# Kernel tuning notes

Hardware: AMD Instinct MI355X
Metric: run time of the kernel (lower is better)

## Reference

```python
import jax, jax.numpy as jnp
import numpy as np

N_EMBED = 768
NUM_HEADS = 12
HEAD_SIZE = N_EMBED // NUM_HEADS
EPS = 1e-6


def layer_norm(x, gamma, beta):
    # torch .var() is unbiased (ddof=1)
    mean = x.mean(-1, keepdims=True)
    var = jnp.var(x, axis=-1, keepdims=True, ddof=1)
    xhat = (x - mean) / jnp.sqrt(var + EPS)
    return gamma * xhat + beta


def setup_inputs() -> dict:
    key = jax.random.key(0)
    ks = jax.random.split(key, 10)
    B, S, D = 4, 2048, N_EMBED
    H = 4 * D
    s = 0.02
    return {
        "x": jax.random.normal(ks[0], (B, S, D), jnp.float32),
        "wq": jax.random.normal(ks[1], (D, D), jnp.float32) * s,
        "wk": jax.random.normal(ks[2], (D, D), jnp.float32) * s,
        "wv": jax.random.normal(ks[3], (D, D), jnp.float32) * s,
        "wo": jax.random.normal(ks[4], (D, D), jnp.float32) * s,
        "w1": jax.random.normal(ks[5], (D, H), jnp.float32) * s,
        "b1": jnp.zeros((H,), jnp.float32),
        "w2": jax.random.normal(ks[6], (H, D), jnp.float32) * s,
        "b2": jnp.zeros((D,), jnp.float32),
        "gamma1": jnp.ones((D,), jnp.float32),
        "beta1": jnp.zeros((D,), jnp.float32),
        "gamma2": jnp.ones((D,), jnp.float32),
        "beta2": jnp.zeros((D,), jnp.float32),
    }


def reference(x, wq, wk, wv, wo, w1, b1, w2, b2, gamma1, beta1, gamma2, beta2):
    B, S, D = x.shape
    Hh, hs = NUM_HEADS, HEAD_SIZE

    # --- pre-LN causal self-attention ---
    xn = layer_norm(x, gamma1, beta1)
    q = (xn @ wq).reshape(B, S, Hh, hs).transpose(0, 2, 1, 3)  # [B,H,S,hs]
    k = (xn @ wk).reshape(B, S, Hh, hs).transpose(0, 2, 1, 3)
    v = (xn @ wv).reshape(B, S, Hh, hs).transpose(0, 2, 1, 3)

    scale = 1.0 / np.sqrt(hs).astype(np.float32)
    scores = jnp.einsum("bhqd,bhkd->bhqk", q, k) * scale  # [B,H,S,S]
    causal = jnp.tril(jnp.ones((S, S), bool))
    scores = jnp.where(causal, scores, -jnp.inf)
    weights = jax.nn.softmax(scores, axis=-1)
    attn = jnp.einsum("bhqk,bhkd->bhqd", weights, v)  # [B,H,S,hs]
    attn = attn.transpose(0, 2, 1, 3).reshape(B, S, D)
    x = x + attn @ wo

    # --- pre-LN MLP ---
    xn = layer_norm(x, gamma2, beta2)
    h = jax.nn.relu(xn @ w1 + b1)
    x = x + (h @ w2 + b2)
    return x
```

## Files before the change

### kernel.cpp

```cpp
#include <hip/hip_runtime.h>
#include <hip/hip_bf16.h>
#include <math.h>

#define BATCH 4
#define SEQ   2048
#define DMODEL 768
#define NHEAD 12
#define HS    64
#define HID   3072
#define NROWS (BATCH*SEQ)
#define QKVN  (3*DMODEL)
#define EPS   1e-6f

typedef __attribute__((ext_vector_type(8))) short bf16x8;
typedef __attribute__((ext_vector_type(4))) float f32x4;

__device__ inline ushort f2b(float f) {
    union { float f; unsigned u; } x; x.f = f;
    unsigned u = x.u;
    unsigned r = (u + 0x7FFFu + ((u >> 16) & 1u)) >> 16;
    return (ushort)r;
}

#define GLDS16(g, l) __builtin_amdgcn_global_load_lds( \
    (const __attribute__((address_space(1))) void*)(g), \
    (__attribute__((address_space(3))) void*)(l), 16, 0, 0)

__global__ __launch_bounds__(256) void convert_w4(const float* __restrict__ p0,
                                                  const float* __restrict__ p1,
                                                  const float* __restrict__ p2,
                                                  const float* __restrict__ p3,
                                                  ushort* __restrict__ out) {
    const float* srcs[4] = { p0, p1, p2, p3 };
    const float* in = srcs[blockIdx.z];
    ushort* dst = out + (size_t)blockIdx.z * DMODEL * DMODEL;
    __shared__ float tile[32][33];
    const int bx = blockIdx.x * 32;
    const int by = blockIdx.y * 32;
    const int tx = threadIdx.x & 31, ty = threadIdx.x >> 5;
    #pragma unroll
    for (int i = 0; i < 32; i += 8)
        tile[ty + i][tx] = in[(size_t)(by + ty + i) * DMODEL + bx + tx];
    __syncthreads();
    #pragma unroll
    for (int i = 0; i < 32; i += 8)
        dst[(size_t)(bx + ty + i) * DMODEL + by + tx] = f2b(tile[tx][ty + i]);
}

__global__ __launch_bounds__(256) void convert_w(const float* __restrict__ in,
                                                 ushort* __restrict__ out,
                                                 int K, int N) {
    __shared__ float tile[32][33];
    const int bx = blockIdx.x * 32;
    const int by = blockIdx.y * 32;
    const int tx = threadIdx.x & 31, ty = threadIdx.x >> 5;
    #pragma unroll
    for (int i = 0; i < 32; i += 8)
        tile[ty + i][tx] = in[(size_t)(by + ty + i) * N + bx + tx];
    __syncthreads();
    #pragma unroll
    for (int i = 0; i < 32; i += 8)
        out[(size_t)(bx + ty + i) * K + by + tx] = f2b(tile[tx][ty + i]);
}

__global__ __launch_bounds__(256) void transpose_v(const ushort* __restrict__ v,
                                                   ushort* __restrict__ vt) {
    const int st = blockIdx.x;
    const int bh = blockIdx.y;
    const int b = bh / NHEAD, h = bh % NHEAD;
    const ushort* src = v + ((size_t)b * SEQ) * QKVN + h * HS;
    ushort* dst = vt + ((size_t)bh * HS) * SEQ;
    __shared__ ushort t[64][65];
    const int col = threadIdx.x & 63;
    const int r0  = (threadIdx.x >> 6) * 16;
    #pragma unroll
    for (int i = 0; i < 16; ++i)
        t[col][r0 + i] = src[(size_t)(st * 64 + r0 + i) * QKVN + col];
    __syncthreads();
    #pragma unroll
    for (int i = 0; i < 16; ++i)
        dst[(size_t)(r0 + i) * SEQ + st * 64 + col] = t[r0 + i][col];
}

__global__ __launch_bounds__(256) void ln_kernel(const float* __restrict__ x,
                                                 const float* __restrict__ gamma,
                                                 const float* __restrict__ beta,
                                                 ushort* __restrict__ out) {
    const int row = blockIdx.x;
    const float* xr = x + (size_t)row * DMODEL;
    float s = 0.f, s2 = 0.f;
    for (int i = threadIdx.x; i < DMODEL; i += 256) {
        float v = xr[i];
        s += v; s2 += v * v;
    }
    for (int off = 32; off > 0; off >>= 1) {
        s  += __shfl_down(s,  off, 64);
        s2 += __shfl_down(s2, off, 64);
    }
    __shared__ float shs[4], shs2[4];
    int wid = threadIdx.x >> 6, lane = threadIdx.x & 63;
    if (lane == 0) { shs[wid] = s; shs2[wid] = s2; }
    __syncthreads();
    __shared__ float smean, srstd;
    if (threadIdx.x == 0) {
        float S  = shs[0] + shs[1] + shs[2] + shs[3];
        float S2 = shs2[0] + shs2[1] + shs2[2] + shs2[3];
        float mean = S / DMODEL;
        float var  = (S2 - DMODEL * mean * mean) / (DMODEL - 1);
        smean = mean;
        srstd = rsqrtf(var + EPS);
    }
    __syncthreads();
    float mean = smean, rstd = srstd;
    ushort* orow = out + (size_t)row * DMODEL;
    for (int i = threadIdx.x; i < DMODEL; i += 256) {
        orow[i] = f2b(gamma[i] * (xr[i] - mean) * rstd + beta[i]);
    }
}

#define GN 128
#define GK 64
#define GM 64
__global__ __launch_bounds__(256, 3) void gemm_mfma(const ushort* __restrict__ A,
                                                    const ushort* __restrict__ Bt,
                                                    const float* __restrict__ bias,
                                                    const float* __restrict__ res,
                                                    float* __restrict__ C,
                                                    ushort* __restrict__ Cb,
                                                    int M, int N, int K, int do_relu,
                                                    int scale_q) {
    __shared__ ushort As[2][GM * GK];
    __shared__ ushort Bs[2][GN * GK];
    const int tid  = threadIdx.x;
    const int lane = tid & 63, wave = tid >> 6;
    const int l16  = lane & 15, quad = lane >> 4;
    const int wr = wave >> 1, wc = wave & 1;

    const int nwg = gridDim.x * gridDim.y;
    int id = blockIdx.y * gridDim.x + blockIdx.x;
    if ((nwg & 7) == 0) {
        const int chunk = nwg >> 3;
        id = (id & 7) * chunk + (id >> 3);
    }
    const int bx = id % gridDim.x;
    const int by = id / gridDim.x;
    const int row0 = by * GM, col0 = bx * GN;

    f32x4 acc[2][4];
    #pragma unroll
    for (int i = 0; i < 2; ++i)
        #pragma unroll
        for (int j = 0; j < 4; ++j) acc[i][j] = (f32x4){0.f, 0.f, 0.f, 0.f};

    const ushort* Asrc[2];
    const ushort* Bsrc[4];
    #pragma unroll
    for (int i = 0; i < 2; ++i) {
        int c = tid + i * 256, m = c >> 3, j = c & 7;
        Asrc[i] = A + (size_t)(row0 + m) * K + (j ^ (m & 7)) * 8;
    }
    #pragma unroll
    for (int i = 0; i < 4; ++i) {
        int c = tid + i * 256, m = c >> 3, j = c & 7;
        Bsrc[i] = Bt + (size_t)(col0 + m) * K + (j ^ (m & 7)) * 8;
    }

    const int nk = K / GK;
    #pragma unroll
    for (int i = 0; i < 2; ++i) GLDS16(Asrc[i], &As[0][(tid + i * 256) * 8]);
    #pragma unroll
    for (int i = 0; i < 4; ++i)  GLDS16(Bsrc[i], &Bs[0][(tid + i * 256) * 8]);

    for (int kt = 0; kt < nk; ++kt) {
        const int p = kt & 1;
        __syncthreads();
        if (kt + 1 < nk) {
            const int k1 = (kt + 1) * GK;
            #pragma unroll
            for (int i = 0; i < 2; ++i) GLDS16(Asrc[i] + k1, &As[p ^ 1][(tid + i * 256) * 8]);
            #pragma unroll
            for (int i = 0; i < 4; ++i)  GLDS16(Bsrc[i] + k1, &Bs[p ^ 1][(tid + i * 256) * 8]);
        }

        #pragma unroll
        for (int s = 0; s < 2; ++s) {
            bf16x8 af[2], bfr[4];
            #pragma unroll
            for (int i = 0; i < 2; ++i) {
                int m = wr * 32 + i * 16 + l16;
                af[i] = *(const bf16x8*)&As[p][(m * 8 + (((s << 2) | quad) ^ (m & 7))) * 8];
            }
            #pragma unroll
            for (int j = 0; j < 4; ++j) {
                int n = wc * 64 + j * 16 + l16;
                bfr[j] = *(const bf16x8*)&Bs[p][(n * 8 + (((s << 2) | quad) ^ (n & 7))) * 8];
            }
            #pragma unroll
            for (int i = 0; i < 2; ++i)
                #pragma unroll
                for (int j = 0; j < 4; ++j)
                    acc[i][j] = __builtin_amdgcn_mfma_f32_16x16x32_bf16(af[i], bfr[j], acc[i][j], 0, 0, 0);
        }
    }

    #pragma unroll
    for (int i = 0; i < 2; ++i) {
        #pragma unroll
        for (int r = 0; r < 4; ++r) {
            int row = row0 + wr * 32 + i * 16 + quad * 4 + r;
            #pragma unroll
            for (int j = 0; j < 4; ++j) {
                int col = col0 + wc * 64 + j * 16 + l16;
                float v = acc[i][j][r];
                if (bias) v += bias[col];
                if (do_relu) v = fmaxf(v, 0.f);
                if (scale_q && col < DMODEL) v *= 0.125f;
                if (res) v += res[(size_t)row * N + col];
                if (Cb) Cb[(size_t)row * N + col] = f2b(v);
                else    C [(size_t)row * N + col] = v;
            }
        }
    }
}

#define TQ 64
#define TK 64
#define PPAD 72
#define NQT (SEQ / TQ)

__global__ __launch_bounds__(256, 3) void fattn_kernel(const ushort* __restrict__ q,
                                                       const ushort* __restrict__ k,
                                                       const ushort* __restrict__ vt,
                                                       ushort* __restrict__ o,
                                                       int ldqkv) {
    const int pair = blockIdx.x;
    const int qts[2] = { pair, NQT - 1 - pair };
    const int bh = blockIdx.y;
    const int b = bh / NHEAD, h = bh % NHEAD;
    const int tid  = threadIdx.x;
    const int wave = tid >> 6;
    const int lane = tid & 63;
    const int l16  = lane & 15;
    const int quad = lane >> 4;

    __shared__ ushort Ks[2][TK * 64];
    __shared__ ushort Vs[2][HS * 64];
    __shared__ ushort Ps[4][16][PPAD];

    const size_t base  = ((size_t)b * SEQ) * ldqkv + (size_t)h * HS;
    const size_t baseO = ((size_t)b * SEQ) * DMODEL + (size_t)h * HS;
    const ushort* vth = vt + ((size_t)bh * HS) * SEQ;

    const int r0 = tid >> 3, j0 = (tid & 7) ^ (r0 & 7);
    const int r1 = (tid + 256) >> 3, j1 = (tid & 7) ^ (r1 & 7);
    const ushort* Ksrc0 = k + base + (size_t)r0 * ldqkv + j0 * 8;
    const ushort* Ksrc1 = k + base + (size_t)r1 * ldqkv + j1 * 8;
    const ushort* Vsrc0 = vth + (size_t)r0 * SEQ + j0 * 8;
    const ushort* Vsrc1 = vth + (size_t)r1 * SEQ + j1 * 8;

    bf16x8 qf[2][2];
    #pragma unroll
    for (int t = 0; t < 2; ++t) {
        int qrow = qts[t] * TQ + wave * 16 + l16;
        const ushort* qp = q + base + (size_t)qrow * ldqkv + quad * 8;
        qf[t][0] = *(const bf16x8*)(qp);
        qf[t][1] = *(const bf16x8*)(qp + 32);
    }

    f32x4 Oacc[2][4];
    float lrow[2][4];
    #pragma unroll
    for (int t = 0; t < 2; ++t) {
        #pragma unroll
        for (int f = 0; f < 4; ++f) Oacc[t][f] = (f32x4){0.f, 0.f, 0.f, 0.f};
        #pragma unroll
        for (int r = 0; r < 4; ++r) lrow[t][r] = 0.f;
    }

    const int ktiles = qts[1] + 1;
    GLDS16(Ksrc0, &Ks[0][tid * 8]);
    GLDS16(Ksrc1, &Ks[0][(tid + 256) * 8]);
    GLDS16(Vsrc0, &Vs[0][tid * 8]);
    GLDS16(Vsrc1, &Vs[0][(tid + 256) * 8]);

    for (int kt = 0; kt < ktiles; ++kt) {
        const int p = kt & 1;
        __syncthreads();
        if (kt + 1 < ktiles) {
            const size_t ko = (size_t)(kt + 1) * TK;
            GLDS16(Ksrc0 + ko * ldqkv, &Ks[p ^ 1][tid * 8]);
            GLDS16(Ksrc1 + ko * ldqkv, &Ks[p ^ 1][(tid + 256) * 8]);
            GLDS16(Vsrc0 + ko,         &Vs[p ^ 1][tid * 8]);
            GLDS16(Vsrc1 + ko,         &Vs[p ^ 1][(tid + 256) * 8]);
        }

        bf16x8 kb[4][2], vb[4][2];
        #pragma unroll
        for (int f = 0; f < 4; ++f) {
            int row = f * 16 + l16;
            kb[f][0] = *(const bf16x8*)&Ks[p][(row * 8 + (quad ^ (row & 7))) * 8];
            kb[f][1] = *(const bf16x8*)&Ks[p][(row * 8 + ((4 | quad) ^ (row & 7))) * 8];
            vb[f][0] = *(const bf16x8*)&Vs[p][(row * 8 + (quad ^ (row & 7))) * 8];
            vb[f][1] = *(const bf16x8*)&Vs[p][(row * 8 + ((4 | quad) ^ (row & 7))) * 8];
        }

        #pragma unroll
        for (int t = 0; t < 2; ++t) {
            const int qt = qts[t];
            if (kt > qt) continue;

            f32x4 S[4];
            #pragma unroll
            for (int f = 0; f < 4; ++f) {
                f32x4 a = (f32x4){0.f, 0.f, 0.f, 0.f};
                a = __builtin_amdgcn_mfma_f32_16x16x32_bf16(qf[t][0], kb[f][0], a, 0, 0, 0);
                a = __builtin_amdgcn_mfma_f32_16x16x32_bf16(qf[t][1], kb[f][1], a, 0, 0, 0);
                S[f] = a;
            }

            const int qrow_base = qt * TQ + wave * 16 + quad * 4;
            if (kt == qt) {
                #pragma unroll
                for (int f = 0; f < 4; ++f) {
                    int key = kt * TK + f * 16 + l16;
                    #pragma unroll
                    for (int r = 0; r < 4; ++r)
                        if (key > qrow_base + r) S[f][r] = -INFINITY;
                }
            }

            #pragma unroll
            for (int f = 0; f < 4; ++f) {
                #pragma unroll
                for (int r = 0; r < 4; ++r) {
                    float pv = __expf(S[f][r]);
                    S[f][r] = pv;
                    lrow[t][r] += pv;
                }
            }

            #pragma unroll
            for (int f = 0; f < 4; ++f)
                #pragma unroll
                for (int r = 0; r < 4; ++r)
                    Ps[wave][quad * 4 + r][f * 16 + l16] = f2b(S[f][r]);

            bf16x8 pa0 = *(const bf16x8*)&Ps[wave][l16][quad * 8];
            bf16x8 pa1 = *(const bf16x8*)&Ps[wave][l16][32 + quad * 8];
            #pragma unroll
            for (int f = 0; f < 4; ++f) {
                Oacc[t][f] = __builtin_amdgcn_mfma_f32_16x16x32_bf16(pa0, vb[f][0], Oacc[t][f], 0, 0, 0);
                Oacc[t][f] = __builtin_amdgcn_mfma_f32_16x16x32_bf16(pa1, vb[f][1], Oacc[t][f], 0, 0, 0);
            }
        }
    }

    #pragma unroll
    for (int t = 0; t < 2; ++t) {
        const int qrow = qts[t] * TQ + wave * 16 + quad * 4;
        #pragma unroll
        for (int r = 0; r < 4; ++r) {
            float l = lrow[t][r];
            #pragma unroll
            for (int m = 1; m < 16; m <<= 1) l += __shfl_xor(l, m, 64);
            float invl = 1.f / l;
            #pragma unroll
            for (int f = 0; f < 4; ++f)
                o[baseO + (size_t)(qrow + r) * DMODEL + f * 16 + l16] = f2b(Oacc[t][f][r] * invl);
        }
    }
}

extern "C" void kernel_launch(void* const* d_in, const int* in_sizes, int n_in,
                              void* d_out, int out_size, void* d_ws, size_t ws_size,
                              hipStream_t stream) {
    const float* x      = (const float*)d_in[0];
    const float* wq     = (const float*)d_in[1];
    const float* wk     = (const float*)d_in[2];
    const float* wv     = (const float*)d_in[3];
    const float* wo     = (const float*)d_in[4];
    const float* w1     = (const float*)d_in[5];
    const float* b1     = (const float*)d_in[6];
    const float* w2     = (const float*)d_in[7];
    const float* b2     = (const float*)d_in[8];
    const float* gamma1 = (const float*)d_in[9];
    const float* beta1  = (const float*)d_in[10];
    const float* gamma2 = (const float*)d_in[11];
    const float* beta2  = (const float*)d_in[12];
    float* out = (float*)d_out;

    char* ws = (char*)d_ws;
    ushort* buf_xn   = (ushort*)ws;
    ushort* buf_attn = buf_xn;
    ushort* buf_qkv  = (ushort*)(ws + 12582912);
    ushort* buf_h    = buf_qkv;
    ushort* w_qkv    = (ushort*)(ws + 12582912 + 50331648);
    ushort* w_ot     = w_qkv + (size_t)QKVN * DMODEL;
    ushort* w_1t     = w_ot + (size_t)DMODEL * DMODEL;
    ushort* w_2t     = w_1t + (size_t)HID * DMODEL;
    ushort* buf_vt   = (ushort*)d_out;

    convert_w4<<<dim3(DMODEL/32, DMODEL/32, 4), 256, 0, stream>>>(wq, wk, wv, wo, w_qkv);
    convert_w<<<dim3(HID/32,    DMODEL/32), 256, 0, stream>>>(w1, w_1t, DMODEL, HID);
    convert_w<<<dim3(DMODEL/32, HID/32),    256, 0, stream>>>(w2, w_2t, HID, DMODEL);

    ln_kernel<<<NROWS, 256, 0, stream>>>(x, gamma1, beta1, buf_xn);
    gemm_mfma<<<dim3(QKVN/GN, NROWS/GM), 256, 0, stream>>>(buf_xn, w_qkv, nullptr, nullptr,
                                                           nullptr, buf_qkv, NROWS, QKVN, DMODEL, 0, 1);
    transpose_v<<<dim3(SEQ/64, BATCH*NHEAD), 256, 0, stream>>>(buf_qkv + 2*DMODEL, buf_vt);
    fattn_kernel<<<dim3(NQT/2, BATCH*NHEAD), 256, 0, stream>>>(buf_qkv, buf_qkv + DMODEL,
                                                               buf_vt, buf_attn, QKVN);
    gemm_mfma<<<dim3(DMODEL/GN, NROWS/GM), 256, 0, stream>>>(buf_attn, w_ot, nullptr, x,
                                                             out, nullptr, NROWS, DMODEL, DMODEL, 0, 0);
    ln_kernel<<<NROWS, 256, 0, stream>>>(out, gamma2, beta2, buf_xn);
    gemm_mfma<<<dim3(HID/GN, NROWS/GM), 256, 0, stream>>>(buf_xn, w_1t, b1, nullptr,
                                                          nullptr, buf_h, NROWS, HID, DMODEL, 1, 0);
    gemm_mfma<<<dim3(DMODEL/GN, NROWS/GM), 256, 0, stream>>>(buf_h, w_2t, b2, out,
                                                             out, nullptr, NROWS, DMODEL, HID, 0, 0);
}
```

Baseline: 413.7 us.

## Add 128x128-tile GEMM kernel with XCD block remap for QKV and FFN1

Adds a new bf16 MFMA GEMM, gemm_big, that computes a 128x128 output tile per workgroup with 4x4 MFMA fragments per wave. It loads into double-buffered, XOR-swizzled LDS and remaps workgroup IDs across the 8 XCDs. The QKV projection and the first MLP GEMM now use it, aiming for more operand reuse and fewer global loads per FLOP. The trade-offs are higher register pressure and fewer workgroups for these large-N GEMMs.

```diff
diff --git a/kernel.cpp b/kernel.cpp
--- a/kernel.cpp
+++ b/kernel.cpp
@@ -223,6 +223,110 @@
     }
 }
 
+#define HM 128
+#define HN 128
+#define HK 32
+__device__ __forceinline__ int sw4(int m) { return (m & 3) ^ ((m >> 2) & 3); }
+
+__global__ __launch_bounds__(256, 4) void gemm_big(const ushort* __restrict__ A,
+                                                   const ushort* __restrict__ Bt,
+                                                   const float* __restrict__ bias,
+                                                   const float* __restrict__ res,
+                                                   float* __restrict__ C,
+                                                   ushort* __restrict__ Cb,
+                                                   int M, int N, int K, int do_relu,
+                                                   int scale_q) {
+    __shared__ ushort As[2][HM * HK];
+    __shared__ ushort Bs[2][HN * HK];
+    const int tid  = threadIdx.x;
+    const int lane = tid & 63, wave = tid >> 6;
+    const int l16  = lane & 15, quad = lane >> 4;
+    const int wr = wave >> 1, wc = wave & 1;
+
+    const int nwg = gridDim.x * gridDim.y;
+    int id = blockIdx.y * gridDim.x + blockIdx.x;
+    if ((nwg & 7) == 0) {
+        const int chunk = nwg >> 3;
+        id = (id & 7) * chunk + (id >> 3);
+    }
+    const int bx = id % gridDim.x;
+    const int by = id / gridDim.x;
+    const int row0 = by * HM, col0 = bx * HN;
+
+    f32x4 acc[4][4];
+    #pragma unroll
+    for (int i = 0; i < 4; ++i)
+        #pragma unroll
+        for (int j = 0; j < 4; ++j) acc[i][j] = (f32x4){0.f, 0.f, 0.f, 0.f};
+
+    const ushort* Asrc[2];
+    const ushort* Bsrc[2];
+    #pragma unroll
+    for (int i = 0; i < 2; ++i) {
+        int c = tid + i * 256, m = c >> 2, jl = c & 3;
+        Asrc[i] = A + (size_t)(row0 + m) * K + (jl ^ sw4(m)) * 8;
+    }
+    #pragma unroll
+    for (int i = 0; i < 2; ++i) {
+        int c = tid + i * 256, m = c >> 2, jl = c & 3;
+        Bsrc[i] = Bt + (size_t)(col0 + m) * K + (jl ^ sw4(m)) * 8;
+    }
+
+    const int nk = K / HK;
+    #pragma unroll
+    for (int i = 0; i < 2; ++i) GLDS16(Asrc[i], &As[0][(tid + i * 256) * 8]);
+    #pragma unroll
+    for (int i = 0; i < 2; ++i) GLDS16(Bsrc[i], &Bs[0][(tid + i * 256) * 8]);
+
+    for (int kt = 0; kt < nk; ++kt) {
+        const int p = kt & 1;
+        __syncthreads();
+        if (kt + 1 < nk) {
+            const int k1 = (kt + 1) * HK;
+            #pragma unroll
+            for (int i = 0; i < 2; ++i) GLDS16(Asrc[i] + k1, &As[p ^ 1][(tid + i * 256) * 8]);
+            #pragma unroll
+            for (int i = 0; i < 2; ++i) GLDS16(Bsrc[i] + k1, &Bs[p ^ 1][(tid + i * 256) * 8]);
+        }
+
+        bf16x8 af[4], bfr[4];
+        #pragma unroll
+        for (int i = 0; i < 4; ++i) {
+            int m = wr * 64 + i * 16 + l16;
+            af[i] = *(const bf16x8*)&As[p][(m * 4 + (quad ^ sw4(m))) * 8];
+        }
+        #pragma unroll
+        for (int j = 0; j < 4; ++j) {
+            int n = wc * 64 + j * 16 + l16;
+            bfr[j] = *(const bf16x8*)&Bs[p][(n * 4 + (quad ^ sw4(n))) * 8];
+        }
+        #pragma unroll
+        for (int i = 0; i < 4; ++i)
+            #pragma unroll
+            for (int j = 0; j < 4; ++j)
+                acc[i][j] = __builtin_amdgcn_mfma_f32_16x16x32_bf16(af[i], bfr[j], acc[i][j], 0, 0, 0);
+    }
+
+    #pragma unroll
+    for (int i = 0; i < 4; ++i) {
+        #pragma unroll
+        for (int r = 0; r < 4; ++r) {
+            int row = row0 + wr * 64 + i * 16 + quad * 4 + r;
+            #pragma unroll
+            for (int j = 0; j < 4; ++j) {
+                int col = col0 + wc * 64 + j * 16 + l16;
+                float v = acc[i][j][r];
+                if (bias) v += bias[col];
+                if (do_relu) v = fmaxf(v, 0.f);
+                if (scale_q && col < DMODEL) v *= 0.125f;
+                if (res) v += res[(size_t)row * N + col];
+                if (Cb) Cb[(size_t)row * N + col] = f2b(v);
+                else    C [(size_t)row * N + col] = v;
+            }
+        }
+    }
+}
+
 #define TQ 64
 #define TK 64
 #define PPAD 72
@@ -405,16 +509,16 @@
     convert_w<<<dim3(DMODEL/32, HID/32),    256, 0, stream>>>(w2, w_2t, HID, DMODEL);
 
     ln_kernel<<<NROWS, 256, 0, stream>>>(x, gamma1, beta1, buf_xn);
-    gemm_mfma<<<dim3(QKVN/GN, NROWS/GM), 256, 0, stream>>>(buf_xn, w_qkv, nullptr, nullptr,
-                                                           nullptr, buf_qkv, NROWS, QKVN, DMODEL, 0, 1);
+    gemm_big<<<dim3(QKVN/HN, NROWS/HM), 256, 0, stream>>>(buf_xn, w_qkv, nullptr, nullptr,
+                                                          nullptr, buf_qkv, NROWS, QKVN, DMODEL, 0, 1);
     transpose_v<<<dim3(SEQ/64, BATCH*NHEAD), 256, 0, stream>>>(buf_qkv + 2*DMODEL, buf_vt);
     fattn_kernel<<<dim3(NQT/2, BATCH*NHEAD), 256, 0, stream>>>(buf_qkv, buf_qkv + DMODEL,
                                                                buf_vt, buf_attn, QKVN);
     gemm_mfma<<<dim3(DMODEL/GN, NROWS/GM), 256, 0, stream>>>(buf_attn, w_ot, nullptr, x,
                                                              out, nullptr, NROWS, DMODEL, DMODEL, 0, 0);
     ln_kernel<<<NROWS, 256, 0, stream>>>(out, gamma2, beta2, buf_xn);
-    gemm_mfma<<<dim3(HID/GN, NROWS/GM), 256, 0, stream>>>(buf_xn, w_1t, b1, nullptr,
-                                                          nullptr, buf_h, NROWS, HID, DMODEL, 1, 0);
+    gemm_big<<<dim3(HID/HN, NROWS/HM), 256, 0, stream>>>(buf_xn, w_1t, b1, nullptr,
+                                                         nullptr, buf_h, NROWS, HID, DMODEL, 1, 0);
     gemm_mfma<<<dim3(DMODEL/GN, NROWS/GM), 256, 0, stream>>>(buf_h, w_2t, b2, out,
                                                              out, nullptr, NROWS, DMODEL, HID, 0, 0);
 }
```

Result: no change. 414.1 us (+0.1%).
